# Kernel tuning notes

Hardware: AMD Instinct MI355X
Metric: run time of the kernel (lower is better)

## Reference

```python
import jax, jax.numpy as jnp
import numpy as np
import math

B, S, D, H = 4, 2048, 1024, 16
HD = D // H


def setup_inputs() -> dict:
    key = jax.random.key(0)
    ks = jax.random.split(key, 12)
    sc = 1.0 / math.sqrt(D)
    inp = {
        "query": jax.random.normal(ks[0], (B, S, D), jnp.float32),
        "key": jax.random.normal(ks[1], (B, S, D), jnp.float32),
        "value": jax.random.normal(ks[2], (B, S, D), jnp.float32),
        "mask": jnp.tril(jnp.ones((S, S), jnp.bool_))[None, None],  # [1,1,S,S] causal
        "wq": jax.random.normal(ks[3], (D, D), jnp.float32) * sc,
        "bq": jax.random.normal(ks[4], (D,), jnp.float32) * sc,
        "wk": jax.random.normal(ks[5], (D, D), jnp.float32) * sc,
        "bk": jax.random.normal(ks[6], (D,), jnp.float32) * sc,
        "wv": jax.random.normal(ks[7], (D, D), jnp.float32) * sc,
        "bv": jax.random.normal(ks[8], (D,), jnp.float32) * sc,
        "wo": jax.random.normal(ks[9], (D, D), jnp.float32) * sc,
        "bo": jax.random.normal(ks[10], (D,), jnp.float32) * sc,
    }
    return inp


def reference(query, key, value, mask, wq, bq, wk, bk, wv, bv, wo, bo):
    # QKV projections (torch Linear: x @ W.T + b)
    q = query @ wq.T + bq
    k = key @ wk.T + bk
    v = value @ wv.T + bv
    # [B,S,D] -> [B,H,S,HD]
    q = q.reshape(B, S, H, HD).transpose(0, 2, 1, 3)
    k = k.reshape(B, S, H, HD).transpose(0, 2, 1, 3)
    v = v.reshape(B, S, H, HD).transpose(0, 2, 1, 3)
    scores = jnp.einsum("bhqd,bhkd->bhqk", q, k) / math.sqrt(HD)
    scores = jnp.where(mask, scores, -jnp.inf)
    weights = jax.nn.softmax(scores, axis=-1)
    attn = jnp.einsum("bhqk,bhkd->bhqd", weights, v)
    attn = attn.transpose(0, 2, 1, 3).reshape(B, S, D)
    return attn @ wo.T + bo
```

## Files before the change

### kernel.cpp

```cpp
#include <hip/hip_runtime.h>
#include <hip/hip_bf16.h>

#define B_  4
#define S_  2048
#define D_  1024
#define H_  16
#define HD_ 64
#define M_  (B_ * S_)

typedef __bf16 bf16x8 __attribute__((ext_vector_type(8)));
typedef float  f32x4  __attribute__((ext_vector_type(4)));
typedef float  f32x16 __attribute__((ext_vector_type(16)));
typedef unsigned int   u32x4 __attribute__((ext_vector_type(4)));
typedef unsigned short u16x8 __attribute__((ext_vector_type(8)));

typedef __attribute__((address_space(1))) const void gv_t;
typedef __attribute__((address_space(3))) void lv_t;

__device__ inline bf16x8 cvt8(float4 a, float4 b) {
    bf16x8 r;
    r[0] = (__bf16)a.x; r[1] = (__bf16)a.y; r[2] = (__bf16)a.z; r[3] = (__bf16)a.w;
    r[4] = (__bf16)b.x; r[5] = (__bf16)b.y; r[6] = (__bf16)b.z; r[7] = (__bf16)b.w;
    return r;
}

__device__ __forceinline__ unsigned pk2(float lo, float hi) {
    unsigned short a = __builtin_bit_cast(unsigned short, (__bf16)lo);
    unsigned short b = __builtin_bit_cast(unsigned short, (__bf16)hi);
    return (unsigned)a | ((unsigned)b << 16);
}

__global__ __launch_bounds__(256) void cvt_w(
    const float* __restrict__ wq, const float* __restrict__ wk,
    const float* __restrict__ wv, const float* __restrict__ wo,
    __bf16* __restrict__ oq, __bf16* __restrict__ ok,
    __bf16* __restrict__ ov, __bf16* __restrict__ oo) {
    const size_t NW = 1048576;
    const size_t step = (size_t)gridDim.x * 256 * 8;
    for (size_t e = ((size_t)blockIdx.x * 256 + threadIdx.x) * 8; e < 4 * NW;
         e += step) {
        const float* s; __bf16* d;
        if (e < NW)            { s = wq + e;          d = oq + e; }
        else if (e < 2 * NW)   { s = wk + (e - NW);   d = ok + (e - NW); }
        else if (e < 3 * NW)   { s = wv + (e - 2*NW); d = ov + (e - 2*NW); }
        else                   { s = wo + (e - 3*NW); d = oo + (e - 3*NW); }
        *(bf16x8*)d = cvt8(*(const float4*)s, *(const float4*)(s + 4));
    }
}

__device__ __forceinline__ void gemm_body_f32A(
    const float* __restrict__ A, const __bf16* __restrict__ Wb,
    const float* __restrict__ bias, __bf16* __restrict__ Y, float out_scale,
    float* Asf, __bf16* Bs) {
    const int K = 1024;
    const int m0 = blockIdx.x * 128, n0 = blockIdx.y * 128;
    const int tid = threadIdx.x;
    const int w = tid >> 6, lane = tid & 63;
    const int wr = (w >> 1) * 64, wc = (w & 1) * 64;
    const int l15 = lane & 15, hi4 = lane >> 4;

    f32x4 acc[4][4] = {};

    const int srow8  = tid >> 3;
    const int sblk8  = tid & 7;
    const int srow16 = tid >> 4;
    const int sblk16 = tid & 15;

    for (int kb = 0; kb < K; kb += 64) {
#pragma unroll
        for (int c = 0; c < 4; ++c) {
            int row = c * 32 + srow8;
            int soff = ((sblk8 ^ (row & 7)) << 4);
            const char* sb = (const char*)(Wb + (size_t)(n0 + row) * K + kb) + soff;
            __builtin_amdgcn_global_load_lds(
                (gv_t*)sb, (lv_t*)((char*)Bs + c * 4096 + tid * 16), 16, 0, 0);
        }
#pragma unroll
        for (int c = 0; c < 8; ++c) {
            int row = c * 16 + srow16;
            int soff = ((sblk16 ^ (row & 15)) << 4);
            const char* sa = (const char*)(A + (size_t)(m0 + row) * K + kb) + soff;
            __builtin_amdgcn_global_load_lds(
                (gv_t*)sa, (lv_t*)((char*)Asf + c * 4096 + tid * 16), 16, 0, 0);
        }
        __syncthreads();
#pragma unroll
        for (int kh = 0; kh < 2; ++kh) {
            bf16x8 af[4], bfr[4];
#pragma unroll
            for (int m = 0; m < 4; ++m) {
                int row = wr + m * 16 + l15;
                const char* base = (const char*)Asf + row * 256;
                int b0 = kh * 8 + hi4 * 2;
                float4 a0 = *(const float4*)(base + ((b0 ^ (row & 15)) << 4));
                float4 a1 = *(const float4*)(base + (((b0 + 1) ^ (row & 15)) << 4));
                af[m] = cvt8(a0, a1);
            }
            const int blk = kh * 4 + hi4;
#pragma unroll
            for (int n = 0; n < 4; ++n) {
                int row = wc + n * 16 + l15;
                bfr[n] = *(const bf16x8*)((const char*)Bs + row * 128 +
                                          ((blk ^ (row & 7)) << 4));
            }
#pragma unroll
            for (int m = 0; m < 4; ++m)
#pragma unroll
                for (int n = 0; n < 4; ++n)
                    acc[m][n] = __builtin_amdgcn_mfma_f32_16x16x32_bf16(
                        af[m], bfr[n], acc[m][n], 0, 0, 0);
        }
        __syncthreads();
    }

#pragma unroll
    for (int n = 0; n < 4; ++n) {
        int col = n0 + wc + n * 16 + l15;
        float bb = bias[col];
#pragma unroll
        for (int m = 0; m < 4; ++m) {
            int rowb = m0 + wr + m * 16 + hi4 * 4;
#pragma unroll
            for (int r = 0; r < 4; ++r) {
                float v = (acc[m][n][r] + bb) * out_scale;
                int row = rowb + r;
                int b = row >> 11, s = row & (S_ - 1);
                int h = col >> 6, hd = col & (HD_ - 1);
                Y[(((size_t)(b * H_ + h)) * S_ + s) * HD_ + hd] = (__bf16)v;
            }
        }
    }
}

__global__ __launch_bounds__(256) void gemm_qkv(
    const float* __restrict__ q, const float* __restrict__ k,
    const float* __restrict__ v, const __bf16* __restrict__ wqb,
    const __bf16* __restrict__ wkb, const __bf16* __restrict__ wvb,
    const float* __restrict__ bq, const float* __restrict__ bk,
    const float* __restrict__ bv, __bf16* __restrict__ oq,
    __bf16* __restrict__ ok, __bf16* __restrict__ ov, float qsc) {
    __shared__ __align__(16) float  Asf[128 * 64];
    __shared__ __align__(16) __bf16 Bs[128 * 64];
    const float *A; const __bf16 *Wb; const float* bias; __bf16* Y; float sc;
    if (blockIdx.z == 0)      { A = q; Wb = wqb; bias = bq; Y = oq; sc = qsc; }
    else if (blockIdx.z == 1) { A = k; Wb = wkb; bias = bk; Y = ok; sc = 1.f; }
    else                      { A = v; Wb = wvb; bias = bv; Y = ov; sc = 1.f; }
    gemm_body_f32A(A, Wb, bias, Y, sc, Asf, Bs);
}

__global__ __launch_bounds__(256) void gemm_o(
    const __bf16* __restrict__ A, const __bf16* __restrict__ Wb,
    const float* __restrict__ bias, float* __restrict__ Y) {
    __shared__ __align__(16) __bf16 As[128 * 64];
    __shared__ __align__(16) __bf16 Bs[128 * 64];
    const int K = 1024, N = 1024;
    const int m0 = blockIdx.x * 128, n0 = blockIdx.y * 128;
    const int tid = threadIdx.x;
    const int w = tid >> 6, lane = tid & 63;
    const int wr = (w >> 1) * 64, wc = (w & 1) * 64;
    const int l15 = lane & 15, hi4 = lane >> 4;

    f32x4 acc[4][4] = {};

    const int srow8 = tid >> 3;
    const int sblk  = tid & 7;

    for (int kb = 0; kb < K; kb += 64) {
#pragma unroll
        for (int c = 0; c < 4; ++c) {
            int row = c * 32 + srow8;
            int soff = ((sblk ^ (row & 7)) << 4);
            const char* sa = (const char*)(A + (size_t)(m0 + row) * K + kb) + soff;
            __builtin_amdgcn_global_load_lds(
                (gv_t*)sa, (lv_t*)((char*)As + c * 4096 + tid * 16), 16, 0, 0);
            const char* sb = (const char*)(Wb + (size_t)(n0 + row) * K + kb) + soff;
            __builtin_amdgcn_global_load_lds(
                (gv_t*)sb, (lv_t*)((char*)Bs + c * 4096 + tid * 16), 16, 0, 0);
        }
        __syncthreads();
#pragma unroll
        for (int kh = 0; kh < 2; ++kh) {
            bf16x8 af[4], bfr[4];
            const int blk = kh * 4 + hi4;
#pragma unroll
            for (int m = 0; m < 4; ++m) {
                int row = wr + m * 16 + l15;
                af[m] = *(const bf16x8*)((const char*)As + row * 128 +
                                         ((blk ^ (row & 7)) << 4));
            }
#pragma unroll
            for (int n = 0; n < 4; ++n) {
                int row = wc + n * 16 + l15;
                bfr[n] = *(const bf16x8*)((const char*)Bs + row * 128 +
                                          ((blk ^ (row & 7)) << 4));
            }
#pragma unroll
            for (int m = 0; m < 4; ++m)
#pragma unroll
                for (int n = 0; n < 4; ++n)
                    acc[m][n] = __builtin_amdgcn_mfma_f32_16x16x32_bf16(
                        af[m], bfr[n], acc[m][n], 0, 0, 0);
        }
        __syncthreads();
    }

#pragma unroll
    for (int n = 0; n < 4; ++n) {
        int col = n0 + wc + n * 16 + l15;
        float bb = bias[col];
#pragma unroll
        for (int m = 0; m < 4; ++m) {
            int rowb = m0 + wr + m * 16 + hi4 * 4;
#pragma unroll
            for (int r = 0; r < 4; ++r)
                Y[(size_t)(rowb + r) * N + col] = acc[m][n][r] + bb;
        }
    }
}

__device__ __forceinline__ void stage_k256(__bf16* kbuf, const __bf16* Kh,
                                           int k0, int tid) {
#pragma unroll
    for (int c = 0; c < 2; ++c) {
        int row = c * 32 + (tid >> 3);
        int blk = (tid & 7) ^ (row & 7);
        const char* src = (const char*)(Kh + (size_t)(k0 + row) * HD_) + blk * 16;
        __builtin_amdgcn_global_load_lds(
            (gv_t*)src, (lv_t*)((char*)kbuf + c * 4096 + tid * 16), 16, 0, 0);
    }
}

__device__ __forceinline__ u16x8 load_v8(const __bf16* Vh, int k0, int vrg,
                                         int vcol) {
    u16x8 r;
#pragma unroll
    for (int j = 0; j < 8; ++j)
        r[j] = *(const unsigned short*)(Vh + (size_t)(k0 + vrg * 8 + j) * HD_ + vcol);
    return r;
}

__device__ __forceinline__ void store_vt(__bf16* vt, u16x8 a, int vcol, int blk) {
    int byt = vcol * 128 + ((blk ^ (vcol & 7)) << 4);
    *(u16x8*)((char*)vt + byt) = a;
}

__global__ __launch_bounds__(256, 2) void attn_fwd(
    const __bf16* __restrict__ Q, const __bf16* __restrict__ K,
    const __bf16* __restrict__ V, __bf16* __restrict__ O) {
    __shared__ __align__(16) __bf16 Kb[3][64 * 64];
    __shared__ __align__(16) __bf16 Vt[2][64 * 64];
    const int bh = blockIdx.x;
    const int qt = 15 - blockIdx.y;
    const int tid = threadIdx.x, w = tid >> 6, lane = tid & 63;
    const int l31 = lane & 31, hi = lane >> 5;
    const size_t base = (size_t)bh * S_ * HD_;
    const __bf16* Qh = Q + base;
    const __bf16* Kh = K + base;
    const __bf16* Vh = V + base;
    const int b = bh >> 4, h = bh & 15;
    const int vcol = tid & 63, vrg = tid >> 6;

    const u32x4 onew = {0x3F803F80u, 0x3F803F80u, 0x3F803F80u, 0x3F803F80u};
    const bf16x8 onef = __builtin_bit_cast(bf16x8, onew);

    const int qb0 = qt * 128;
    const int NS = 2 * qt + 2;
    const int qw0 = qb0 + w * 32;
    const int qrow = qw0 + l31;

    bf16x8 qf[4];
#pragma unroll
    for (int sl = 0; sl < 4; ++sl)
        qf[sl] = *(const bf16x8*)(Qh + (size_t)qrow * HD_ + sl * 16 + hi * 8);

    f32x16 accO[2] = {};
    f32x16 accL = {};

    u16x8 va = load_v8(Vh, 0, vrg, vcol);
    u16x8 vb = load_v8(Vh, 32, vrg, vcol);
    __builtin_amdgcn_sched_barrier(0);
    stage_k256(&Kb[0][0], Kh, 0, tid);
    stage_k256(&Kb[1][0], Kh, 64, tid);
    __builtin_amdgcn_sched_barrier(0);
    asm volatile("s_waitcnt vmcnt(2)" ::: "memory");
    __builtin_amdgcn_sched_barrier(0);
    store_vt(&Vt[0][0], va, vcol, vrg);
    store_vt(&Vt[0][0], vb, vcol, vrg + 4);
    asm volatile("s_waitcnt lgkmcnt(0)" ::: "memory");
    __builtin_amdgcn_sched_barrier(0);
    __builtin_amdgcn_s_barrier();
    __builtin_amdgcn_sched_barrier(0);

    for (int s = 0; s < NS; ++s) {
        const int k0 = s * 64;
        const int tV = (s + 1 < NS) ? s + 1 : NS - 1;
        const int tK = (s + 2 < NS) ? s + 2 : NS - 1;
        u16x8 nva = load_v8(Vh, tV * 64, vrg, vcol);
        u16x8 nvb = load_v8(Vh, tV * 64 + 32, vrg, vcol);
        __builtin_amdgcn_sched_barrier(0);
        stage_k256(&Kb[(s + 2) % 3][0], Kh, tK * 64, tid);
        __builtin_amdgcn_sched_barrier(0);

        const bool active = (k0 <= qw0 + 31);
        if (active) {
            const char* kbuf = (const char*)&Kb[s % 3][0];
            const char* vbuf = (const char*)&Vt[s & 1][0];
            f32x16 sc[2] = {};
            __builtin_amdgcn_s_setprio(1);
#pragma unroll
            for (int sub = 0; sub < 2; ++sub)
#pragma unroll
                for (int sl = 0; sl < 4; ++sl) {
                    int row = sub * 32 + l31;
                    int byt = row * 128 + (((2 * sl + hi) ^ (row & 7)) << 4);
                    bf16x8 kf = *(const bf16x8*)(kbuf + byt);
                    sc[sub] = __builtin_amdgcn_mfma_f32_32x32x16_bf16(
                        kf, qf[sl], sc[sub], 0, 0, 0);
                }
            __builtin_amdgcn_s_setprio(0);
            if (k0 + 64 > qw0) {
#pragma unroll
                for (int sub = 0; sub < 2; ++sub)
#pragma unroll
                    for (int r = 0; r < 16; ++r) {
                        int k = k0 + 32 * sub + (r & 3) + 8 * (r >> 2) + 4 * hi;
                        if (k > qrow) sc[sub][r] = -3.0e38f;
                    }
            }
#pragma unroll
            for (int sub = 0; sub < 2; ++sub)
#pragma unroll
                for (int r = 0; r < 16; ++r)
                    sc[sub][r] = __builtin_amdgcn_exp2f(sc[sub][r]);
            bf16x8 pa[4];
#pragma unroll
            for (int sl = 0; sl < 4; ++sl) {
                const int sub = sl >> 1, rb = 8 * (sl & 1);
                u32x4 wds = {pk2(sc[sub][rb + 0], sc[sub][rb + 1]),
                             pk2(sc[sub][rb + 2], sc[sub][rb + 3]),
                             pk2(sc[sub][rb + 4], sc[sub][rb + 5]),
                             pk2(sc[sub][rb + 6], sc[sub][rb + 7])};
                pa[sl] = __builtin_bit_cast(bf16x8, wds);
            }
            __builtin_amdgcn_s_setprio(1);
#pragma unroll
            for (int t = 0; t < 2; ++t)
#pragma unroll
                for (int sl = 0; sl < 4; ++sl) {
                    int row = t * 32 + l31;
                    const char* vbp = vbuf + row * 128 + hi * 8;
                    uint2 lo = *(const uint2*)(vbp + (((2 * sl) ^ (row & 7)) << 4));
                    uint2 hw = *(const uint2*)(vbp + (((2 * sl + 1) ^ (row & 7)) << 4));
                    u32x4 vv = {lo.x, lo.y, hw.x, hw.y};
                    bf16x8 vf = __builtin_bit_cast(bf16x8, vv);
                    accO[t] = __builtin_amdgcn_mfma_f32_32x32x16_bf16(
                        vf, pa[sl], accO[t], 0, 0, 0);
                }
#pragma unroll
            for (int sl = 0; sl < 4; ++sl)
                accL = __builtin_amdgcn_mfma_f32_32x32x16_bf16(
                    onef, pa[sl], accL, 0, 0, 0);
            __builtin_amdgcn_s_setprio(0);
        }
        asm volatile("s_waitcnt vmcnt(2)" ::: "memory");
        __builtin_amdgcn_sched_barrier(0);
        store_vt(&Vt[(s + 1) & 1][0], nva, vcol, vrg);
        store_vt(&Vt[(s + 1) & 1][0], nvb, vcol, vrg + 4);
        asm volatile("s_waitcnt lgkmcnt(0)" ::: "memory");
        __builtin_amdgcn_sched_barrier(0);
        __builtin_amdgcn_s_barrier();
        __builtin_amdgcn_sched_barrier(0);
    }

    float inv = 1.0f / accL[0];
    __bf16* orow = O + ((size_t)b * S_ + qrow) * D_ + h * HD_;
#pragma unroll
    for (int t = 0; t < 2; ++t)
#pragma unroll
        for (int g = 0; g < 4; ++g) {
            unsigned w0 = pk2(accO[t][4 * g + 0] * inv, accO[t][4 * g + 1] * inv);
            unsigned w1 = pk2(accO[t][4 * g + 2] * inv, accO[t][4 * g + 3] * inv);
            uint2 u = {w0, w1};
            *(uint2*)(orow + t * 32 + g * 8 + hi * 4) = u;
        }
}

extern "C" void kernel_launch(void* const* d_in, const int* in_sizes, int n_in,
                              void* d_out, int out_size, void* d_ws, size_t ws_size,
                              hipStream_t stream) {
    const float* query = (const float*)d_in[0];
    const float* key_  = (const float*)d_in[1];
    const float* value = (const float*)d_in[2];
    const float* wq = (const float*)d_in[4];
    const float* bq = (const float*)d_in[5];
    const float* wk = (const float*)d_in[6];
    const float* bk = (const float*)d_in[7];
    const float* wv = (const float*)d_in[8];
    const float* bv = (const float*)d_in[9];
    const float* wo = (const float*)d_in[10];
    const float* bo = (const float*)d_in[11];
    float* out = (float*)d_out;

    const float QSC = 0.125f * 1.44269504088896341f;

    const size_t SZ = (size_t)M_ * D_ * 2;
    const size_t WB = (size_t)D_ * D_ * 2;
    char* wsb = (char*)d_ws;
    __bf16* qws = (__bf16*)(wsb + 0 * SZ);
    __bf16* kws = (__bf16*)(wsb + 1 * SZ);
    __bf16* vws = (__bf16*)(wsb + 2 * SZ);
    __bf16* aws = (__bf16*)(wsb + 3 * SZ);
    __bf16* bwq = (__bf16*)(wsb + 4 * SZ);
    __bf16* bwk = (__bf16*)(wsb + 4 * SZ + 1 * WB);
    __bf16* bwv = (__bf16*)(wsb + 4 * SZ + 2 * WB);
    __bf16* bwo = (__bf16*)(wsb + 4 * SZ + 3 * WB);

    dim3 bb(256);
    hipLaunchKernelGGL(cvt_w, dim3(512), bb, 0, stream,
                       wq, wk, wv, wo, bwq, bwk, bwv, bwo);
    hipLaunchKernelGGL(gemm_qkv, dim3(M_ / 128, D_ / 128, 3), bb, 0, stream,
                       query, key_, value, bwq, bwk, bwv, bq, bk, bv,
                       qws, kws, vws, QSC);
    hipLaunchKernelGGL(attn_fwd, dim3(B_ * H_, 16), bb, 0, stream,
                       qws, kws, vws, aws);
    hipLaunchKernelGGL(gemm_o, dim3(M_ / 128, D_ / 128), bb, 0, stream,
                       aws, bwo, bo, out);
}
```

Before: 174.3 us.

## Double-buffer weight tiles and read fp32 activations directly from global in QKV GEMM

The QKV projection kernel no longer stages the fp32 activation tile in LDS. Each wave now loads its A fragments straight from global memory and converts them to bf16 in registers. The weight tile is double-buffered in LDS, so the next k-step's weights are prefetched while the current step runs, and one barrier per iteration is dropped. This cuts LDS traffic and per-block shared memory, which may help occupancy. In exchange, A rows are re-read from global by both column-half waves and the loads are less coalesced.

```diff
diff --git a/kernel.cpp b/kernel.cpp
--- a/kernel.cpp
+++ b/kernel.cpp
@@ -48,90 +48,6 @@
     }
 }
 
-__device__ __forceinline__ void gemm_body_f32A(
-    const float* __restrict__ A, const __bf16* __restrict__ Wb,
-    const float* __restrict__ bias, __bf16* __restrict__ Y, float out_scale,
-    float* Asf, __bf16* Bs) {
-    const int K = 1024;
-    const int m0 = blockIdx.x * 128, n0 = blockIdx.y * 128;
-    const int tid = threadIdx.x;
-    const int w = tid >> 6, lane = tid & 63;
-    const int wr = (w >> 1) * 64, wc = (w & 1) * 64;
-    const int l15 = lane & 15, hi4 = lane >> 4;
-
-    f32x4 acc[4][4] = {};
-
-    const int srow8  = tid >> 3;
-    const int sblk8  = tid & 7;
-    const int srow16 = tid >> 4;
-    const int sblk16 = tid & 15;
-
-    for (int kb = 0; kb < K; kb += 64) {
-#pragma unroll
-        for (int c = 0; c < 4; ++c) {
-            int row = c * 32 + srow8;
-            int soff = ((sblk8 ^ (row & 7)) << 4);
-            const char* sb = (const char*)(Wb + (size_t)(n0 + row) * K + kb) + soff;
-            __builtin_amdgcn_global_load_lds(
-                (gv_t*)sb, (lv_t*)((char*)Bs + c * 4096 + tid * 16), 16, 0, 0);
-        }
-#pragma unroll
-        for (int c = 0; c < 8; ++c) {
-            int row = c * 16 + srow16;
-            int soff = ((sblk16 ^ (row & 15)) << 4);
-            const char* sa = (const char*)(A + (size_t)(m0 + row) * K + kb) + soff;
-            __builtin_amdgcn_global_load_lds(
-                (gv_t*)sa, (lv_t*)((char*)Asf + c * 4096 + tid * 16), 16, 0, 0);
-        }
-        __syncthreads();
-#pragma unroll
-        for (int kh = 0; kh < 2; ++kh) {
-            bf16x8 af[4], bfr[4];
-#pragma unroll
-            for (int m = 0; m < 4; ++m) {
-                int row = wr + m * 16 + l15;
-                const char* base = (const char*)Asf + row * 256;
-                int b0 = kh * 8 + hi4 * 2;
-                float4 a0 = *(const float4*)(base + ((b0 ^ (row & 15)) << 4));
-                float4 a1 = *(const float4*)(base + (((b0 + 1) ^ (row & 15)) << 4));
-                af[m] = cvt8(a0, a1);
-            }
-            const int blk = kh * 4 + hi4;
-#pragma unroll
-            for (int n = 0; n < 4; ++n) {
-                int row = wc + n * 16 + l15;
-                bfr[n] = *(const bf16x8*)((const char*)Bs + row * 128 +
-                                          ((blk ^ (row & 7)) << 4));
-            }
-#pragma unroll
-            for (int m = 0; m < 4; ++m)
-#pragma unroll
-                for (int n = 0; n < 4; ++n)
-                    acc[m][n] = __builtin_amdgcn_mfma_f32_16x16x32_bf16(
-                        af[m], bfr[n], acc[m][n], 0, 0, 0);
-        }
-        __syncthreads();
-    }
-
-#pragma unroll
-    for (int n = 0; n < 4; ++n) {
-        int col = n0 + wc + n * 16 + l15;
-        float bb = bias[col];
-#pragma unroll
-        for (int m = 0; m < 4; ++m) {
-            int rowb = m0 + wr + m * 16 + hi4 * 4;
-#pragma unroll
-            for (int r = 0; r < 4; ++r) {
-                float v = (acc[m][n][r] + bb) * out_scale;
-                int row = rowb + r;
-                int b = row >> 11, s = row & (S_ - 1);
-                int h = col >> 6, hd = col & (HD_ - 1);
-                Y[(((size_t)(b * H_ + h)) * S_ + s) * HD_ + hd] = (__bf16)v;
-            }
-        }
-    }
-}
-
 __global__ __launch_bounds__(256) void gemm_qkv(
     const float* __restrict__ q, const float* __restrict__ k,
     const float* __restrict__ v, const __bf16* __restrict__ wqb,
@@ -139,13 +55,86 @@
     const float* __restrict__ bq, const float* __restrict__ bk,
     const float* __restrict__ bv, __bf16* __restrict__ oq,
     __bf16* __restrict__ ok, __bf16* __restrict__ ov, float qsc) {
-    __shared__ __align__(16) float  Asf[128 * 64];
-    __shared__ __align__(16) __bf16 Bs[128 * 64];
+    __shared__ __align__(16) __bf16 Bs[2][128 * 64];
     const float *A; const __bf16 *Wb; const float* bias; __bf16* Y; float sc;
     if (blockIdx.z == 0)      { A = q; Wb = wqb; bias = bq; Y = oq; sc = qsc; }
     else if (blockIdx.z == 1) { A = k; Wb = wkb; bias = bk; Y = ok; sc = 1.f; }
     else                      { A = v; Wb = wvb; bias = bv; Y = ov; sc = 1.f; }
-    gemm_body_f32A(A, Wb, bias, Y, sc, Asf, Bs);
+
+    const int K = 1024;
+    const int m0 = blockIdx.x * 128, n0 = blockIdx.y * 128;
+    const int tid = threadIdx.x;
+    const int w = tid >> 6, lane = tid & 63;
+    const int wr = (w >> 1) * 64, wc = (w & 1) * 64;
+    const int l15 = lane & 15, hi4 = lane >> 4;
+
+    f32x4 acc[4][4] = {};
+
+    const int srow8 = tid >> 3;
+    const int sblk  = tid & 7;
+
+    auto stage_b = [&](int kb, int buf) {
+#pragma unroll
+        for (int c = 0; c < 4; ++c) {
+            int row = c * 32 + srow8;
+            int soff = ((sblk ^ (row & 7)) << 4);
+            const char* sb = (const char*)(Wb + (size_t)(n0 + row) * K + kb) + soff;
+            __builtin_amdgcn_global_load_lds(
+                (gv_t*)sb, (lv_t*)((char*)&Bs[buf][0] + c * 4096 + tid * 16),
+                16, 0, 0);
+        }
+    };
+
+    stage_b(0, 0);
+    __syncthreads();
+
+    for (int s = 0; s < 16; ++s) {
+        const int kb = s * 64;
+        if (s + 1 < 16) stage_b(kb + 64, (s + 1) & 1);
+        __builtin_amdgcn_sched_barrier(0);
+        const char* bsb = (const char*)&Bs[s & 1][0];
+#pragma unroll
+        for (int kh = 0; kh < 2; ++kh) {
+            bf16x8 af[4], bfr[4];
+#pragma unroll
+            for (int m = 0; m < 4; ++m) {
+                const float* ap =
+                    A + (size_t)(m0 + wr + m * 16 + l15) * K + kb + kh * 32 + hi4 * 8;
+                af[m] = cvt8(*(const float4*)ap, *(const float4*)(ap + 4));
+            }
+            const int blk = kh * 4 + hi4;
+#pragma unroll
+            for (int n = 0; n < 4; ++n) {
+                int row = wc + n * 16 + l15;
+                bfr[n] = *(const bf16x8*)(bsb + row * 128 + ((blk ^ (row & 7)) << 4));
+            }
+#pragma unroll
+            for (int m = 0; m < 4; ++m)
+#pragma unroll
+                for (int n = 0; n < 4; ++n)
+                    acc[m][n] = __builtin_amdgcn_mfma_f32_16x16x32_bf16(
+                        af[m], bfr[n], acc[m][n], 0, 0, 0);
+        }
+        __syncthreads();
+    }
+
+#pragma unroll
+    for (int n = 0; n < 4; ++n) {
+        int col = n0 + wc + n * 16 + l15;
+        float bb = bias[col];
+#pragma unroll
+        for (int m = 0; m < 4; ++m) {
+            int rowb = m0 + wr + m * 16 + hi4 * 4;
+#pragma unroll
+            for (int r = 0; r < 4; ++r) {
+                float vv = (acc[m][n][r] + bb) * sc;
+                int row = rowb + r;
+                int b = row >> 11, ss = row & (S_ - 1);
+                int h = col >> 6, hd = col & (HD_ - 1);
+                Y[(((size_t)(b * H_ + h)) * S_ + ss) * HD_ + hd] = (__bf16)vv;
+            }
+        }
+    }
 }
 
 __global__ __launch_bounds__(256) void gemm_o(
```

After: 284.4 us. 1.63x slower.
